# Kernel tuning notes

Hardware: AMD Instinct MI355X
Metric: run time of the kernel (lower is better)

Reference implementation:

```python
import jax, jax.numpy as jnp
import numpy as np

BETA = 0.9
ITER = 2


def setup_inputs() -> dict:
    key = jax.random.key(0)
    B, items, E = 8, 32, 128
    N = B * items * items  # 8192 pairs
    k1, k2 = jax.random.split(key)
    pairs = jax.random.normal(k1, (N, E), dtype=jnp.float32)
    # scale W so bilinear scores don't saturate sigmoid (init faithfulness not required)
    W = jax.random.normal(k2, (E, E), dtype=jnp.float32) / jnp.sqrt(jnp.float32(E))
    cond = jnp.ones((B, items, items), dtype=jnp.int32)  # all pairs valid (dense nonzero)
    # map_pair[b,i,j] = row-major linear index into `pairs`, matching torch.nonzero order
    map_pair = jnp.arange(N, dtype=jnp.int32).reshape(B, items, items)
    return {"pairs": pairs, "W": W, "cond": cond, "map_pair": map_pair}


def reference(pairs, W, cond, map_pair):
    B, items = map_pair.shape[0], map_pair.shape[1]
    N, E = pairs.shape
    # torch.nonzero of the broadcast [B,items,items,items] cond; cond is dense (all nonzero),
    # so nonzeros enumerate all (b,i,j,k) in row-major order.
    bi, ii, ji, ki = [x.reshape(-1) for x in jnp.indices((B, items, items, items))]
    part1 = map_pair[bi, ii, ki]  # pair (i,k)
    part2 = map_pair[bi, ki, ji]  # pair (k,j)
    valid = (part1 >= 0) & (part2 >= 0)  # [N*items]
    # static -inf masks (loop-invariant)
    eq_mask = ((ji == ki) | (ii == ki)).reshape(N, items)  # idx2==idx3 or idx1==idx3
    ar = jnp.arange(items)
    diag_idx = map_pair[:, ar, ar].reshape(-1)  # self-pairs (i,i) -> rows of N
    row_mask = jnp.zeros((N,), dtype=bool).at[diag_idx].set(True)
    inf_mask = eq_mask | row_mask[:, None]  # [N, items]
    neg_inf = jnp.float32(-jnp.inf)

    for _ in range(ITER):
        # generate: bilinear then gather
        bilin = pairs @ W  # [N, E]
        a = jnp.where(valid[:, None], bilin[part1], 0.0).reshape(N, items, E)
        b = jnp.where(valid[:, None], pairs[part2], 0.0).reshape(N, items, E)
        new_pairs = a * b  # [N, items, E]
        # aggregate: masked -inf fills
        new_pairs = jnp.where(inf_mask[:, :, None], neg_inf, new_pairs)
        zero_mask = jnp.all(new_pairs == 0.0, axis=2)  # [N, items]
        new_pairs = jnp.where(zero_mask[:, :, None], neg_inf, new_pairs)
        # interpolation gate: 1 where all walks are masked, beta otherwise
        mat = jnp.where(jnp.all(jnp.isinf(new_pairs), axis=1), 1.0, jnp.float32(BETA))  # [N, E]
        new = jnp.sum(jax.nn.sigmoid(new_pairs), axis=1)  # sigmoid(-inf)=0; [N, E]
        pairs = mat * pairs + (1.0 - mat) * new
    return pairs
```

## Files before the change

### kernel.cpp

```cpp
#include <hip/hip_runtime.h>

typedef __attribute__((ext_vector_type(8))) short bf16x8;
typedef __attribute__((ext_vector_type(4))) float f32x4;

__device__ __forceinline__ short f2bf(float f) {
    unsigned u = __float_as_uint(f);
    unsigned r = (u + 0x7FFFu + ((u >> 16) & 1u)) >> 16;
    return (short)r;
}

__global__ __launch_bounds__(512, 4) void walk_iter(
    const float* __restrict__ src,
    const float* __restrict__ W,
    float* __restrict__ dst)
{
    __shared__ short Wt[128][136];
    __shared__ short Abf[32][136];
    __shared__ float G[32][132];

    const int t  = threadIdx.x;
    const int bi = blockIdx.x >> 1;
    const int jg = blockIdx.x & 1;
    const int b  = bi >> 5;
    const int i  = bi & 31;

    #pragma unroll
    for (int q = 0; q < 8; ++q) {
        int f = t + 512 * q;
        int k = f >> 5, n0 = (f & 31) << 2;
        float4 v = *(const float4*)(W + (size_t)f * 4);
        Wt[n0 + 0][k] = f2bf(v.x);
        Wt[n0 + 1][k] = f2bf(v.y);
        Wt[n0 + 2][k] = f2bf(v.z);
        Wt[n0 + 3][k] = f2bf(v.w);
    }
    {
        const float4* s4 = (const float4*)(src + (size_t)bi * 4096);
        #pragma unroll
        for (int q = 0; q < 2; ++q) {
            int f = t + 512 * q;
            float4 v = s4[f];
            int r = f >> 5, c = (f & 31) << 2;
            union { short s[4]; unsigned long long u; } pk;
            pk.s[0] = f2bf(v.x); pk.s[1] = f2bf(v.y);
            pk.s[2] = f2bf(v.z); pk.s[3] = f2bf(v.w);
            *(unsigned long long*)&Abf[r][c] = pk.u;
        }
    }
    __syncthreads();

    {
        const int wv = t >> 6, l = t & 63;
        const int m0 = (wv & 1) * 16;
        const int lm = l & 15, quad = l >> 4;
        #pragma unroll
        for (int half = 0; half < 2; ++half) {
            const int n0 = ((wv >> 1) + half * 4) * 16;
            f32x4 acc = {0.f, 0.f, 0.f, 0.f};
            #pragma unroll
            for (int kb = 0; kb < 4; ++kb) {
                int ko = kb * 32 + quad * 8;
                bf16x8 af = *(const bf16x8*)&Abf[m0 + lm][ko];
                bf16x8 bf = *(const bf16x8*)&Wt[n0 + lm][ko];
                acc = __builtin_amdgcn_mfma_f32_16x16x32_bf16(af, bf, acc, 0, 0, 0);
            }
            #pragma unroll
            for (int r = 0; r < 4; ++r)
                G[m0 + quad * 4 + r][n0 + lm] = acc[r];
        }
    }
    __syncthreads();

    const int j = jg * 16 + (t >> 5);
    const int g = t & 31, e0 = g << 2;
    float4 sacc = make_float4(0.f, 0.f, 0.f, 0.f);

    if (i != j) {
        const float* pb = src + ((size_t)(b * 32) * 32 + j) * 128 + e0;
        #pragma unroll 4
        for (int k = 0; k < 32; ++k, pb += 4096) {
            if (k == i) continue;
            if (k == j) continue;
            float4 p  = *(const float4*)pb;
            float4 gg = *(const float4*)&G[k][e0];
            float x0 = gg.x * p.x, x1 = gg.y * p.y;
            float x2 = gg.z * p.z, x3 = gg.w * p.w;
            float d0 = 1.0f + __expf(-x0);
            float d1 = 1.0f + __expf(-x1);
            float d2 = 1.0f + __expf(-x2);
            float d3 = 1.0f + __expf(-x3);
            float r01 = __builtin_amdgcn_rcpf(d0 * d1);
            float r23 = __builtin_amdgcn_rcpf(d2 * d3);
            sacc.x += r01 * d1;
            sacc.y += r01 * d0;
            sacc.z += r23 * d3;
            sacc.w += r23 * d2;
        }
    }

    const float matv = (i == j) ? 1.0f : 0.9f;
    const float om   = 1.0f - matv;
    const size_t orow = ((size_t)bi * 32 + j) * 128 + e0;
    float4 pr = *(const float4*)(src + orow);
    float4 o  = make_float4(matv * pr.x + om * sacc.x,
                            matv * pr.y + om * sacc.y,
                            matv * pr.z + om * sacc.z,
                            matv * pr.w + om * sacc.w);
    *(float4*)(dst + orow) = o;
}

extern "C" void kernel_launch(void* const* d_in, const int* in_sizes, int n_in,
                              void* d_out, int out_size, void* d_ws, size_t ws_size,
                              hipStream_t stream) {
    (void)in_sizes; (void)n_in; (void)out_size; (void)ws_size;
    const float* pairs = (const float*)d_in[0];
    const float* W     = (const float*)d_in[1];
    float* tmp = (float*)d_ws;
    float* out = (float*)d_out;

    walk_iter<<<512, 512, 0, stream>>>(pairs, W, tmp);
    walk_iter<<<512, 512, 0, stream>>>(tmp,   W, out);
}
```

Baseline: 103.8 us.

## Precompute bf16 operands in a prep kernel and stream MFMA inputs from global

Adds a prep kernel that converts W (pre-scaled by -log2e and transposed) and the input pairs to bf16 once. Each walk_iter then reads its MFMA operands straight from global memory instead of converting W in shared memory per block, and writes a bf16 copy of its output for the next iteration. The sigmoid inner loop is rewritten to use exp2 with one reciprocal per four elements, branch-free masking, and software prefetch of the next pair row. The cost is an extra launch and extra workspace traffic, in exchange for less LDS usage and higher occupancy.

```diff
diff --git a/kernel.cpp b/kernel.cpp
--- a/kernel.cpp
+++ b/kernel.cpp
@@ -2,6 +2,8 @@
 
 typedef __attribute__((ext_vector_type(8))) short bf16x8;
 typedef __attribute__((ext_vector_type(4))) float f32x4;
+
+#define NEG_LOG2E (-1.4426950408889634f)
 
 __device__ __forceinline__ short f2bf(float f) {
     unsigned u = __float_as_uint(f);
@@ -9,13 +11,34 @@
     return (short)r;
 }
 
-__global__ __launch_bounds__(512, 4) void walk_iter(
-    const float* __restrict__ src,
+__global__ __launch_bounds__(256) void prep(
+    const float* __restrict__ pairs,
     const float* __restrict__ W,
-    float* __restrict__ dst)
+    short* __restrict__ pbf,
+    short* __restrict__ WTs)
 {
-    __shared__ short Wt[128][136];
-    __shared__ short Abf[32][136];
+    const int t = threadIdx.x, blk = blockIdx.x;
+    if (blk < 64) {
+        int idx = blk * 256 + t;
+        int k = idx >> 7, n = idx & 127;
+        WTs[n * 128 + k] = f2bf(NEG_LOG2E * W[idx]);
+    } else {
+        int f = (blk - 64) * 256 + t;
+        float4 v = ((const float4*)pairs)[f];
+        union { short s[4]; unsigned long long u; } pk;
+        pk.s[0] = f2bf(v.x); pk.s[1] = f2bf(v.y);
+        pk.s[2] = f2bf(v.z); pk.s[3] = f2bf(v.w);
+        *(unsigned long long*)(pbf + (size_t)f * 4) = pk.u;
+    }
+}
+
+__global__ __launch_bounds__(512, 6) void walk_iter(
+    const float* __restrict__ srcF,
+    const short* __restrict__ srcB,
+    const short* __restrict__ WTs,
+    float* __restrict__ dstF,
+    short* __restrict__ dstB)
+{
     __shared__ float G[32][132];
 
     const int t  = threadIdx.x;
@@ -24,89 +47,84 @@
     const int b  = bi >> 5;
     const int i  = bi & 31;
 
-    #pragma unroll
-    for (int q = 0; q < 8; ++q) {
-        int f = t + 512 * q;
-        int k = f >> 5, n0 = (f & 31) << 2;
-        float4 v = *(const float4*)(W + (size_t)f * 4);
-        Wt[n0 + 0][k] = f2bf(v.x);
-        Wt[n0 + 1][k] = f2bf(v.y);
-        Wt[n0 + 2][k] = f2bf(v.z);
-        Wt[n0 + 3][k] = f2bf(v.w);
-    }
-    {
-        const float4* s4 = (const float4*)(src + (size_t)bi * 4096);
-        #pragma unroll
-        for (int q = 0; q < 2; ++q) {
-            int f = t + 512 * q;
-            float4 v = s4[f];
-            int r = f >> 5, c = (f & 31) << 2;
-            union { short s[4]; unsigned long long u; } pk;
-            pk.s[0] = f2bf(v.x); pk.s[1] = f2bf(v.y);
-            pk.s[2] = f2bf(v.z); pk.s[3] = f2bf(v.w);
-            *(unsigned long long*)&Abf[r][c] = pk.u;
-        }
-    }
-    __syncthreads();
+    const int j  = jg * 16 + (t >> 5);
+    const int g  = t & 31, e0 = g << 2;
+
+    const float* pb = srcF + ((size_t)(b * 32) * 32 + j) * 128 + e0;
+    float4 pA = *(const float4*)pb;
 
     {
         const int wv = t >> 6, l = t & 63;
         const int m0 = (wv & 1) * 16;
         const int lm = l & 15, quad = l >> 4;
+        const int n0 = (wv >> 1) * 16;
+        const short* arow = srcB + (size_t)(bi * 32 + m0 + lm) * 128;
+        const short* brow = WTs + (size_t)(n0 + lm) * 128;
+        f32x4 acc0 = {0.f, 0.f, 0.f, 0.f};
+        f32x4 acc1 = {0.f, 0.f, 0.f, 0.f};
         #pragma unroll
-        for (int half = 0; half < 2; ++half) {
-            const int n0 = ((wv >> 1) + half * 4) * 16;
-            f32x4 acc = {0.f, 0.f, 0.f, 0.f};
-            #pragma unroll
-            for (int kb = 0; kb < 4; ++kb) {
-                int ko = kb * 32 + quad * 8;
-                bf16x8 af = *(const bf16x8*)&Abf[m0 + lm][ko];
-                bf16x8 bf = *(const bf16x8*)&Wt[n0 + lm][ko];
-                acc = __builtin_amdgcn_mfma_f32_16x16x32_bf16(af, bf, acc, 0, 0, 0);
-            }
-            #pragma unroll
-            for (int r = 0; r < 4; ++r)
-                G[m0 + quad * 4 + r][n0 + lm] = acc[r];
+        for (int kb = 0; kb < 4; ++kb) {
+            int ko = kb * 32 + quad * 8;
+            bf16x8 af  = *(const bf16x8*)(arow + ko);
+            bf16x8 bf0 = *(const bf16x8*)(brow + ko);
+            bf16x8 bf1 = *(const bf16x8*)(brow + 64 * 128 + ko);
+            acc0 = __builtin_amdgcn_mfma_f32_16x16x32_bf16(af, bf0, acc0, 0, 0, 0);
+            acc1 = __builtin_amdgcn_mfma_f32_16x16x32_bf16(af, bf1, acc1, 0, 0, 0);
+        }
+        #pragma unroll
+        for (int r = 0; r < 4; ++r) {
+            G[m0 + quad * 4 + r][n0 + lm]      = acc0[r];
+            G[m0 + quad * 4 + r][n0 + 64 + lm] = acc1[r];
         }
     }
     __syncthreads();
 
-    const int j = jg * 16 + (t >> 5);
-    const int g = t & 31, e0 = g << 2;
     float4 sacc = make_float4(0.f, 0.f, 0.f, 0.f);
-
     if (i != j) {
-        const float* pb = src + ((size_t)(b * 32) * 32 + j) * 128 + e0;
+        const float* pn = pb + 4096;
+        float4 pB = *(const float4*)pn;
         #pragma unroll 4
-        for (int k = 0; k < 32; ++k, pb += 4096) {
-            if (k == i) continue;
-            if (k == j) continue;
-            float4 p  = *(const float4*)pb;
+        for (int k = 0; k < 32; ++k) {
+            float4 p = pA;
+            pA = pB;
+            if (k < 30) { pn += 4096; pB = *(const float4*)pn; }
             float4 gg = *(const float4*)&G[k][e0];
-            float x0 = gg.x * p.x, x1 = gg.y * p.y;
-            float x2 = gg.z * p.z, x3 = gg.w * p.w;
-            float d0 = 1.0f + __expf(-x0);
-            float d1 = 1.0f + __expf(-x1);
-            float d2 = 1.0f + __expf(-x2);
-            float d3 = 1.0f + __expf(-x3);
-            float r01 = __builtin_amdgcn_rcpf(d0 * d1);
-            float r23 = __builtin_amdgcn_rcpf(d2 * d3);
-            sacc.x += r01 * d1;
-            sacc.y += r01 * d0;
-            sacc.z += r23 * d3;
-            sacc.w += r23 * d2;
+            float t0 = gg.x * p.x, t1 = gg.y * p.y;
+            float t2 = gg.z * p.z, t3 = gg.w * p.w;
+            float x0 = __builtin_amdgcn_exp2f(t0);
+            float x1 = __builtin_amdgcn_exp2f(t1);
+            float x2 = __builtin_amdgcn_exp2f(t2);
+            float x3 = __builtin_amdgcn_exp2f(t3);
+            float d0 = 1.0f + x0, d1 = 1.0f + x1;
+            float d2 = 1.0f + x2, d3 = 1.0f + x3;
+            float d01 = d0 * d1, d23 = d2 * d3;
+            float r = __builtin_amdgcn_rcpf(d01 * d23);
+            r = ((k == i) | (k == j)) ? 0.0f : r;
+            float r01 = r * d23, r23 = r * d01;
+            sacc.x = fmaf(r01, d1, sacc.x);
+            sacc.y = fmaf(r01, d0, sacc.y);
+            sacc.z = fmaf(r23, d3, sacc.z);
+            sacc.w = fmaf(r23, d2, sacc.w);
         }
     }
 
     const float matv = (i == j) ? 1.0f : 0.9f;
     const float om   = 1.0f - matv;
     const size_t orow = ((size_t)bi * 32 + j) * 128 + e0;
-    float4 pr = *(const float4*)(src + orow);
-    float4 o  = make_float4(matv * pr.x + om * sacc.x,
-                            matv * pr.y + om * sacc.y,
-                            matv * pr.z + om * sacc.z,
-                            matv * pr.w + om * sacc.w);
-    *(float4*)(dst + orow) = o;
+    float4 pr = *(const float4*)(srcF + orow);
+    float4 o;
+    o.x = fmaf(om, sacc.x, matv * pr.x);
+    o.y = fmaf(om, sacc.y, matv * pr.y);
+    o.z = fmaf(om, sacc.z, matv * pr.z);
+    o.w = fmaf(om, sacc.w, matv * pr.w);
+    *(float4*)(dstF + orow) = o;
+
+    if (dstB) {
+        union { short s[4]; unsigned long long u; } pk;
+        pk.s[0] = f2bf(o.x); pk.s[1] = f2bf(o.y);
+        pk.s[2] = f2bf(o.z); pk.s[3] = f2bf(o.w);
+        *(unsigned long long*)(dstB + orow) = pk.u;
+    }
 }
 
 extern "C" void kernel_launch(void* const* d_in, const int* in_sizes, int n_in,
@@ -115,9 +133,14 @@
     (void)in_sizes; (void)n_in; (void)out_size; (void)ws_size;
     const float* pairs = (const float*)d_in[0];
     const float* W     = (const float*)d_in[1];
-    float* tmp = (float*)d_ws;
+    char* ws = (char*)d_ws;
+    short* WTs   = (short*)ws;
+    short* pbf   = (short*)(ws + (1 << 16));
+    float* tmp   = (float*)(ws + (1 << 16) + (1 << 21));
+    short* tmpbf = (short*)(ws + (1 << 16) + (1 << 21) + (1 << 22));
     float* out = (float*)d_out;
 
-    walk_iter<<<512, 512, 0, stream>>>(pairs, W, tmp);
-    walk_iter<<<512, 512, 0, stream>>>(tmp,   W, out);
+    prep<<<1088, 256, 0, stream>>>(pairs, W, pbf, WTs);
+    walk_iter<<<512, 512, 0, stream>>>(pairs, pbf, WTs, tmp, tmpbf);
+    walk_iter<<<512, 512, 0, stream>>>(tmp,   tmpbf, WTs, out, nullptr);
 }
```

New measurement: 94.92 us. 8.5% less time.

## Split fused walk kernel into separate GEMM and walk kernels per iteration

Applied to the files above, without the earlier changes.

Splits each iteration into a bilinear GEMM kernel that writes G = pairs@W to global workspace and a separate walk kernel that computes the sigmoid sum. This removes the duplicated per-block W transpose and GEMM (previously two blocks per bi each recomputed it) and raises occupancy with smaller blocks and a 2-wide element mapping. It also folds -log2(e) into W so the walk uses exp2 directly, replaces the skip branches with a select, and software-prefetches the next k. The cost is four launches instead of two and an extra round trip of G through global memory.

```diff
diff --git a/kernel.cpp b/kernel.cpp
--- a/kernel.cpp
+++ b/kernel.cpp
@@ -2,6 +2,8 @@
 
 typedef __attribute__((ext_vector_type(8))) short bf16x8;
 typedef __attribute__((ext_vector_type(4))) float f32x4;
+
+#define NEG_LOG2E (-1.4426950408889634f)
 
 __device__ __forceinline__ short f2bf(float f) {
     unsigned u = __float_as_uint(f);
@@ -9,30 +11,26 @@
     return (short)r;
 }
 
-__global__ __launch_bounds__(512, 4) void walk_iter(
+__global__ __launch_bounds__(512) void gemm_g(
     const float* __restrict__ src,
     const float* __restrict__ W,
-    float* __restrict__ dst)
+    float* __restrict__ G)
 {
     __shared__ short Wt[128][136];
     __shared__ short Abf[32][136];
-    __shared__ float G[32][132];
 
     const int t  = threadIdx.x;
-    const int bi = blockIdx.x >> 1;
-    const int jg = blockIdx.x & 1;
-    const int b  = bi >> 5;
-    const int i  = bi & 31;
+    const int bi = blockIdx.x;
 
     #pragma unroll
     for (int q = 0; q < 8; ++q) {
         int f = t + 512 * q;
         int k = f >> 5, n0 = (f & 31) << 2;
         float4 v = *(const float4*)(W + (size_t)f * 4);
-        Wt[n0 + 0][k] = f2bf(v.x);
-        Wt[n0 + 1][k] = f2bf(v.y);
-        Wt[n0 + 2][k] = f2bf(v.z);
-        Wt[n0 + 3][k] = f2bf(v.w);
+        Wt[n0 + 0][k] = f2bf(NEG_LOG2E * v.x);
+        Wt[n0 + 1][k] = f2bf(NEG_LOG2E * v.y);
+        Wt[n0 + 2][k] = f2bf(NEG_LOG2E * v.z);
+        Wt[n0 + 3][k] = f2bf(NEG_LOG2E * v.w);
     }
     {
         const float4* s4 = (const float4*)(src + (size_t)bi * 4096);
@@ -49,64 +47,70 @@
     }
     __syncthreads();
 
-    {
-        const int wv = t >> 6, l = t & 63;
-        const int m0 = (wv & 1) * 16;
-        const int lm = l & 15, quad = l >> 4;
+    const int wv = t >> 6, l = t & 63;
+    const int m0 = (wv & 1) * 16;
+    const int lm = l & 15, quad = l >> 4;
+    #pragma unroll
+    for (int half = 0; half < 2; ++half) {
+        const int n0 = ((wv >> 1) + half * 4) * 16;
+        f32x4 acc = {0.f, 0.f, 0.f, 0.f};
         #pragma unroll
-        for (int half = 0; half < 2; ++half) {
-            const int n0 = ((wv >> 1) + half * 4) * 16;
-            f32x4 acc = {0.f, 0.f, 0.f, 0.f};
-            #pragma unroll
-            for (int kb = 0; kb < 4; ++kb) {
-                int ko = kb * 32 + quad * 8;
-                bf16x8 af = *(const bf16x8*)&Abf[m0 + lm][ko];
-                bf16x8 bf = *(const bf16x8*)&Wt[n0 + lm][ko];
-                acc = __builtin_amdgcn_mfma_f32_16x16x32_bf16(af, bf, acc, 0, 0, 0);
-            }
-            #pragma unroll
-            for (int r = 0; r < 4; ++r)
-                G[m0 + quad * 4 + r][n0 + lm] = acc[r];
+        for (int kb = 0; kb < 4; ++kb) {
+            int ko = kb * 32 + quad * 8;
+            bf16x8 af = *(const bf16x8*)&Abf[m0 + lm][ko];
+            bf16x8 bf = *(const bf16x8*)&Wt[n0 + lm][ko];
+            acc = __builtin_amdgcn_mfma_f32_16x16x32_bf16(af, bf, acc, 0, 0, 0);
         }
+        #pragma unroll
+        for (int r = 0; r < 4; ++r)
+            G[((size_t)bi * 32 + m0 + quad * 4 + r) * 128 + n0 + lm] = acc[r];
     }
-    __syncthreads();
+}
 
-    const int j = jg * 16 + (t >> 5);
-    const int g = t & 31, e0 = g << 2;
-    float4 sacc = make_float4(0.f, 0.f, 0.f, 0.f);
+__global__ __launch_bounds__(256, 8) void walk(
+    const float* __restrict__ src,
+    const float* __restrict__ G,
+    float* __restrict__ dst)
+{
+    const int blk = (blockIdx.x & 7) * 256 + (blockIdx.x >> 3);
+    const int t   = threadIdx.x;
+    const int row = blk * 4 + (t >> 6);
+    const int l   = t & 63, e0 = l << 1;
+    const int b = row >> 10, i = (row >> 5) & 31, j = row & 31;
 
-    if (i != j) {
-        const float* pb = src + ((size_t)(b * 32) * 32 + j) * 128 + e0;
-        #pragma unroll 4
-        for (int k = 0; k < 32; ++k, pb += 4096) {
-            if (k == i) continue;
-            if (k == j) continue;
-            float4 p  = *(const float4*)pb;
-            float4 gg = *(const float4*)&G[k][e0];
-            float x0 = gg.x * p.x, x1 = gg.y * p.y;
-            float x2 = gg.z * p.z, x3 = gg.w * p.w;
-            float d0 = 1.0f + __expf(-x0);
-            float d1 = 1.0f + __expf(-x1);
-            float d2 = 1.0f + __expf(-x2);
-            float d3 = 1.0f + __expf(-x3);
-            float r01 = __builtin_amdgcn_rcpf(d0 * d1);
-            float r23 = __builtin_amdgcn_rcpf(d2 * d3);
-            sacc.x += r01 * d1;
-            sacc.y += r01 * d0;
-            sacc.z += r23 * d3;
-            sacc.w += r23 * d2;
+    const float* pP = src + ((((size_t)b << 10) + j) << 7) + e0;
+    const float* pG = G + (((size_t)(row >> 5)) << 12) + e0;
+
+    float2 p0 = *(const float2*)pP;
+    float2 g0 = *(const float2*)pG;
+    float sx = 0.f, sy = 0.f;
+
+    #pragma unroll 4
+    for (int k = 0; k < 32; ++k) {
+        float2 p = p0, g = g0;
+        if (k < 31) {
+            pP += 4096; pG += 128;
+            p0 = *(const float2*)pP;
+            g0 = *(const float2*)pG;
         }
+        float t0 = g.x * p.x, t1 = g.y * p.y;
+        float x0 = __builtin_amdgcn_exp2f(t0);
+        float x1 = __builtin_amdgcn_exp2f(t1);
+        float d0 = 1.0f + x0, d1 = 1.0f + x1;
+        float rr = __builtin_amdgcn_rcpf(d0 * d1);
+        rr = ((k == i) | (k == j)) ? 0.0f : rr;
+        sx = fmaf(rr, d1, sx);
+        sy = fmaf(rr, d0, sy);
     }
 
     const float matv = (i == j) ? 1.0f : 0.9f;
     const float om   = 1.0f - matv;
-    const size_t orow = ((size_t)bi * 32 + j) * 128 + e0;
-    float4 pr = *(const float4*)(src + orow);
-    float4 o  = make_float4(matv * pr.x + om * sacc.x,
-                            matv * pr.y + om * sacc.y,
-                            matv * pr.z + om * sacc.z,
-                            matv * pr.w + om * sacc.w);
-    *(float4*)(dst + orow) = o;
+    const size_t orow = (size_t)row * 128 + e0;
+    float2 pr = *(const float2*)(src + orow);
+    float2 o;
+    o.x = fmaf(om, sx, matv * pr.x);
+    o.y = fmaf(om, sy, matv * pr.y);
+    *(float2*)(dst + orow) = o;
 }
 
 extern "C" void kernel_launch(void* const* d_in, const int* in_sizes, int n_in,
@@ -115,9 +119,13 @@
     (void)in_sizes; (void)n_in; (void)out_size; (void)ws_size;
     const float* pairs = (const float*)d_in[0];
     const float* W     = (const float*)d_in[1];
-    float* tmp = (float*)d_ws;
+    char* ws = (char*)d_ws;
+    float* G   = (float*)ws;
+    float* tmp = (float*)(ws + (1 << 22));
     float* out = (float*)d_out;
 
-    walk_iter<<<512, 512, 0, stream>>>(pairs, W, tmp);
-    walk_iter<<<512, 512, 0, stream>>>(tmp,   W, out);
+    gemm_g<<<256, 512, 0, stream>>>(pairs, W, G);
+    walk  <<<2048, 256, 0, stream>>>(pairs, G, tmp);
+    gemm_g<<<256, 512, 0, stream>>>(tmp, W, G);
+    walk  <<<2048, 256, 0, stream>>>(tmp, G, out);
 }
```

Result: slower. 109.5 us (+5.5%).
